# Kernel tuning notes

Measured on AMD Instinct MI355X. Metric: run time of the kernel, lower is better.

Reference implementation:

```python
import jax, jax.numpy as jnp
import numpy as np

V_NUM = 4
NUM_HEADS = 8


def setup_inputs() -> dict:
    key = jax.random.key(0)
    k1, k2, k3 = jax.random.split(key, 3)
    B, C, H, W = 8, 512, 24, 24
    x = jax.random.normal(k1, (B, C, H, W), dtype=jnp.float32)
    # 1x1 conv weights stored as [out_ch, in_ch]
    w_qkv = jax.random.normal(k2, (3 * C, C), dtype=jnp.float32) * (C ** -0.5)
    w_proj = jax.random.normal(k3, (C, C), dtype=jnp.float32) * (C ** -0.5)
    b_proj = jnp.zeros((C,), dtype=jnp.float32)
    return {"x": x, "w_qkv": w_qkv, "w_proj": w_proj, "b_proj": b_proj}


def reference(x, w_qkv, w_proj, b_proj):
    B, C, H, W = x.shape
    hd = C // NUM_HEADS          # head dim
    scale = hd ** -0.5
    g = B // V_NUM               # batch groups
    N = V_NUM * H * W            # tokens per group

    # 1x1 conv qkv (no bias): [B, 3C, H, W]
    qkv = jnp.einsum('bchw,oc->bohw', x, w_qkv)
    # [g, v, 3C, H, W] -> [g, 3C, v, H, W] -> [g, heads, 3*hd, N]
    t = qkv.reshape(g, V_NUM, 3 * C, H, W).transpose(0, 2, 1, 3, 4)
    t = t.reshape(g, NUM_HEADS, 3 * hd, N)
    q, k, v = jnp.split(t, 3, axis=2)  # each [g, heads, hd, N]

    # attn = k^T @ q * scale : [g, heads, N, N]
    attn = jnp.einsum('ghdn,ghdm->ghnm', k, q) * scale
    attn = jax.nn.softmax(attn, axis=-2)  # softmax over the k axis (dim=-2)

    # out = v @ attn : [g, heads, hd, N]
    out = jnp.einsum('ghdn,ghnm->ghdm', v, attn)
    # [g, C, v, H, W] -> [g, v, C, H, W] -> [B, C, H, W]
    out = out.reshape(g, C, V_NUM, H, W).transpose(0, 2, 1, 3, 4).reshape(B, C, H, W)

    # 1x1 conv proj with bias
    out = jnp.einsum('bchw,oc->bohw', out, w_proj) + b_proj[None, :, None, None]
    return out
```

## Files before the change

kernel.cpp:

```cpp
#include <hip/hip_runtime.h>
#include <stdint.h>

typedef _Float16 f16;
typedef _Float16 half8 __attribute__((ext_vector_type(8)));
typedef _Float16 half4 __attribute__((ext_vector_type(4)));
typedef float floatx4 __attribute__((ext_vector_type(4)));

#define LOG2E 1.44269504088896340736f

__device__ __forceinline__ void async_cp16(const void* g, void* l) {
  __builtin_amdgcn_global_load_lds((const __attribute__((address_space(1))) void*)g,
                                   (__attribute__((address_space(3))) void*)l, 16, 0, 0);
}

__global__ __launch_bounds__(256) void k_prep(const float* __restrict__ x,
                                              f16* __restrict__ XT,
                                              const float* __restrict__ wqkv,
                                              const float* __restrict__ wproj,
                                              f16* __restrict__ WQ, f16* __restrict__ WP) {
  __shared__ f16 sT[64][72];
  const int bid = blockIdx.x;
  const int tid = threadIdx.x;
  if (bid < 576) {
    const int hw0 = (bid % 9) * 64, c0 = ((bid / 9) & 7) * 64, b = bid / 72;
    const int cc = tid >> 6, hwc = tid & 63;
    const float* xb = x + (size_t)b * 294912;
    for (int i = 0; i < 16; ++i) {
      int c = c0 + i * 4 + cc;
      sT[hwc][i * 4 + cc] = (f16)xb[c * 576 + hw0 + hwc];
    }
    __syncthreads();
    const int c_c = tid & 63, rr = tid >> 6;
    f16* xtb = XT + ((size_t)b * 576 + hw0) * 512 + c0;
    for (int j = 0; j < 16; ++j) {
      int r = j * 4 + rr;
      xtb[(size_t)r * 512 + c_c] = sT[r][c_c];
    }
  } else {
    const float SCALE_Q = 0.125f * LOG2E;
    const int total1 = 1536 * 512, total2 = 512 * 512;
    for (int idx = (bid - 576) * 256 + tid; idx < total1 + total2; idx += 128 * 256) {
      if (idx < total1) {
        int row = idx >> 9;
        float v = wqkv[idx];
        if ((row % 192) < 64) v *= SCALE_Q;
        WQ[idx] = (f16)v;
      } else {
        WP[idx - total1] = (f16)wproj[idx - total1];
      }
    }
  }
}

__global__ __launch_bounds__(256) void k_qkv_gemm(const f16* __restrict__ XT,
                                                  const f16* __restrict__ WQ,
                                                  f16* __restrict__ Qh, f16* __restrict__ Kh,
                                                  f16* __restrict__ Vh) {
  const int t0 = blockIdx.x * 128, n0 = blockIdx.y * 128;
  __shared__ alignas(16) f16 smem[2 * 128 * 64];
  f16* sA = smem;
  f16* sB = smem + 128 * 64;
  const int tid = threadIdx.x;
  const int wave = tid >> 6, lane = tid & 63, quad = lane >> 4, l16 = lane & 15;
  const int msub = (wave & 1) * 64, nsub = (wave >> 1) * 64;
  const floatx4 fzero = {0.f, 0.f, 0.f, 0.f};
  floatx4 acc[4][4];
  for (int i = 0; i < 4; ++i)
    for (int j = 0; j < 4; ++j) acc[i][j] = fzero;

  for (int k0 = 0; k0 < 512; k0 += 64) {
    __syncthreads();
    for (int p = 0; p < 4; ++p) {
      int e = p * 256 + tid;
      int row = e >> 3, colb = e & 7;
      async_cp16((const char*)XT + ((size_t)(t0 + row) * 512 + k0 + colb * 8) * 2,
                 (char*)sA + e * 16);
      async_cp16((const char*)WQ + ((size_t)(n0 + row) * 512 + k0 + colb * 8) * 2,
                 (char*)sB + e * 16);
    }
    __syncthreads();
    for (int f = 0; f < 2; ++f) {
      half8 a[4], bfr[4];
      for (int ms = 0; ms < 4; ++ms)
        a[ms] = *(const half8*)&sA[(msub + ms * 16 + l16) * 64 + f * 32 + quad * 8];
      for (int ns = 0; ns < 4; ++ns)
        bfr[ns] = *(const half8*)&sB[(nsub + ns * 16 + l16) * 64 + f * 32 + quad * 8];
      for (int ms = 0; ms < 4; ++ms)
        for (int ns = 0; ns < 4; ++ns)
          acc[ms][ns] =
              __builtin_amdgcn_mfma_f32_16x16x32_f16(a[ms], bfr[ns], acc[ms][ns], 0, 0, 0);
    }
  }
  for (int ms = 0; ms < 4; ++ms) {
    int tbase = t0 + msub + ms * 16 + quad * 4;
    for (int ns = 0; ns < 4; ++ns) {
      int row = n0 + nsub + ns * 16 + l16;
      int h = row / 192, rr2 = row % 192;
      int sel = rr2 >> 6, d = rr2 & 63;
      if (sel == 2) continue;
      for (int r = 0; r < 4; ++r) {
        int t = tbase + r;
        int b = t / 576, hw = t % 576;
        int g = b >> 2, v = b & 3;
        int n = v * 576 + hw;
        int gh = g * 8 + h;
        f16 hv = (f16)acc[ms][ns][r];
        size_t idx = ((size_t)gh * 2304 + n) * 64 + d;
        if (sel == 0)
          Qh[idx] = hv;
        else
          Kh[idx] = hv;
      }
    }
  }
  const int r0 = n0 % 192;
  if (r0 != 0) {
    const int vloc = (r0 == 128) ? 0 : 64;
    const int h = (n0 + vloc) / 192;
    f16* sVT = smem;
    __syncthreads();
    if ((wave >> 1) == (vloc >> 6)) {
      for (int ms = 0; ms < 4; ++ms) {
        int tok = msub + ms * 16 + quad * 4;
        for (int ns = 0; ns < 4; ++ns) {
          int d = ns * 16 + l16;
          half4 hv;
          for (int r = 0; r < 4; ++r) hv[r] = (f16)acc[ms][ns][r];
          *(half4*)&sVT[d * 136 + tok] = hv;
        }
      }
    }
    __syncthreads();
    for (int pss = 0; pss < 4; ++pss) {
      int d = pss * 16 + (tid >> 4), chunk = tid & 15;
      int t = t0 + chunk * 8;
      int b = t / 576, hw = t - b * 576;
      int gh = (b >> 2) * 8 + h, n = (b & 3) * 576 + hw;
      *(half8*)(Vh + (size_t)gh * 147456 + (size_t)d * 2304 + n) =
          *(const half8*)&sVT[d * 136 + chunk * 8];
    }
  }
}

__global__ __launch_bounds__(256) void k_attn(const f16* __restrict__ Qh,
                                              const f16* __restrict__ Kh,
                                              const f16* __restrict__ Vh,
                                              f16* __restrict__ AOT) {
  const int mt = blockIdx.x, gh = blockIdx.y;
  const int m0 = mt * 64;
  const int g = gh >> 3, h = gh & 7;
  const f16* Qg = Qh + (size_t)gh * 147456;
  const f16* Kg = Kh + (size_t)gh * 147456;
  const f16* Vg = Vh + (size_t)gh * 147456;
  __shared__ alignas(16) f16 sK[2][2][64 * 64];
  __shared__ alignas(16) f16 sV[2][2][64 * 64];
  const int tid = threadIdx.x;
  const int wave = tid >> 6, lane = tid & 63, quad = lane >> 4, l16 = lane & 15;
  const int wq = wave & 1, half = wave >> 1;
  const floatx4 fzero = {0.f, 0.f, 0.f, 0.f};
  const int sw = l16 & 7;

  auto stage_kv = [&](int ktile, int buf) {
#pragma unroll
    for (int p = 0; p < 8; ++p) {
      const int half_t = (p >> 1) & 1, isV = p >> 2;
      int idx = (p & 1) * 256 + tid;
      int row = idx >> 3, cb = idx & 7, sc = ((cb ^ (row & 7)) << 3);
      int nb = half_t * 1152 + ktile * 64;
      if (!isV)
        async_cp16(Kg + (size_t)(nb + row) * 64 + sc, (char*)&sK[half_t][buf][0] + idx * 16);
      else
        async_cp16(Vg + (size_t)row * 2304 + nb + sc, (char*)&sV[half_t][buf][0] + idx * 16);
    }
  };

  half8 qa[2][2];
  for (int s = 0; s < 2; ++s) {
    int qrow = m0 + wq * 32 + s * 16 + l16;
    qa[s][0] = *(const half8*)(Qg + (size_t)qrow * 64 + quad * 8);
    qa[s][1] = *(const half8*)(Qg + (size_t)qrow * 64 + 32 + quad * 8);
  }

  stage_kv(0, 0);
  __syncthreads();
  stage_kv(1, 1);

  float l_lane[2] = {0.f, 0.f};
  floatx4 o[2][4];
  for (int s = 0; s < 2; ++s)
    for (int dt = 0; dt < 4; ++dt) o[s][dt] = fzero;

  for (int kt = 0; kt < 18; ++kt) {
    const f16* bK = &sK[half][kt & 1][0];
    const f16* bV = &sV[half][kt & 1][0];

    half4 pf[2][4];
#pragma unroll
    for (int nt = 0; nt < 4; ++nt) {
      int krow = nt * 16 + l16;
      half8 kb0 = *(const half8*)&bK[krow * 64 + ((quad ^ sw) << 3)];
      half8 kb1 = *(const half8*)&bK[krow * 64 + (((4 + quad) ^ sw) << 3)];
#pragma unroll
      for (int s = 0; s < 2; ++s) {
        floatx4 t = __builtin_amdgcn_mfma_f32_16x16x32_f16(kb0, qa[s][0], fzero, 0, 0, 0);
        t = __builtin_amdgcn_mfma_f32_16x16x32_f16(kb1, qa[s][1], t, 0, 0, 0);
#pragma unroll
        for (int r = 0; r < 4; ++r) {
          float e = __builtin_amdgcn_exp2f(t[r]);
          l_lane[s] += e;
          pf[s][nt][r] = (f16)e;
        }
      }
    }
#pragma unroll
    for (int dt = 0; dt < 4; ++dt) {
      int vrow = dt * 16 + l16;
#pragma unroll
      for (int nt = 0; nt < 4; ++nt) {
        int chunk = nt * 2 + (quad >> 1);
        half4 vb = *(const half4*)&bV[vrow * 64 + ((chunk ^ sw) << 3) + (quad & 1) * 4];
#pragma unroll
        for (int s = 0; s < 2; ++s)
          o[s][dt] = __builtin_amdgcn_mfma_f32_16x16x16f16(pf[s][nt], vb, o[s][dt], 0, 0, 0);
      }
    }

    if (kt < 17) {
      __syncthreads();
      if (kt + 2 < 18) stage_kv(kt + 2, kt & 1);
    }
  }

  __syncthreads();
  float* cO = (float*)sK;
  float* cL = (float*)sV;
  if (half == 1) {
    for (int s = 0; s < 2; ++s) {
      cL[(wq * 2 + s) * 64 + lane] = l_lane[s];
      for (int dt = 0; dt < 4; ++dt)
        *(floatx4*)&cO[((((wq * 2 + s) * 4 + dt) * 64 + lane) * 4)] = o[s][dt];
    }
  }
  __syncthreads();
  if (half == 0) {
    for (int s = 0; s < 2; ++s) {
      l_lane[s] += cL[(wq * 2 + s) * 64 + lane];
      for (int dt = 0; dt < 4; ++dt)
        o[s][dt] += *(const floatx4*)&cO[((((wq * 2 + s) * 4 + dt) * 64 + lane) * 4)];
    }
    for (int s = 0; s < 2; ++s) {
      l_lane[s] += __shfl_xor(l_lane[s], 16, 64);
      l_lane[s] += __shfl_xor(l_lane[s], 32, 64);
      float inv[4];
      for (int r = 0; r < 4; ++r) {
        float lr = __shfl(l_lane[s], quad * 4 + r, 64);
        inv[r] = 1.f / lr;
      }
      for (int dt = 0; dt < 4; ++dt)
        for (int r = 0; r < 4; ++r) {
          int n_tok = m0 + wq * 32 + s * 16 + quad * 4 + r;
          int v = n_tok / 576, hw = n_tok % 576;
          int bb = g * 4 + v;
          int c = h * 64 + dt * 16 + l16;
          AOT[((size_t)bb * 576 + hw) * 512 + c] = (f16)(o[s][dt][r] * inv[r]);
        }
    }
  }
}

__global__ __launch_bounds__(256) void k_proj_gemm(const f16* __restrict__ AOT,
                                                   const f16* __restrict__ WP,
                                                   const float* __restrict__ bias,
                                                   float* __restrict__ out) {
  const int o0 = blockIdx.x * 64, t0 = blockIdx.y * 128;
  __shared__ alignas(16) f16 sA[64 * 64];
  __shared__ alignas(16) f16 sB[128 * 64];
  const int tid = threadIdx.x;
  const int wave = tid >> 6, lane = tid & 63, quad = lane >> 4, l16 = lane & 15;
  const int msub = (wave & 1) * 32, nsub = (wave >> 1) * 64;
  const floatx4 fzero = {0.f, 0.f, 0.f, 0.f};
  floatx4 acc[2][4];
  for (int i = 0; i < 2; ++i)
    for (int j = 0; j < 4; ++j) acc[i][j] = fzero;

  for (int k0 = 0; k0 < 512; k0 += 64) {
    __syncthreads();
    for (int p = 0; p < 2; ++p) {
      int e = p * 256 + tid;
      int row = e >> 3, colb = e & 7;
      async_cp16((const char*)WP + ((size_t)(o0 + row) * 512 + k0 + colb * 8) * 2,
                 (char*)sA + e * 16);
    }
    for (int p = 0; p < 4; ++p) {
      int e = p * 256 + tid;
      int row = e >> 3, colb = e & 7;
      async_cp16((const char*)AOT + ((size_t)(t0 + row) * 512 + k0 + colb * 8) * 2,
                 (char*)sB + e * 16);
    }
    __syncthreads();
    for (int f = 0; f < 2; ++f) {
      half8 a[2], bfr[4];
      for (int ms = 0; ms < 2; ++ms)
        a[ms] = *(const half8*)&sA[(msub + ms * 16 + l16) * 64 + f * 32 + quad * 8];
      for (int ns = 0; ns < 4; ++ns)
        bfr[ns] = *(const half8*)&sB[(nsub + ns * 16 + l16) * 64 + f * 32 + quad * 8];
      for (int ms = 0; ms < 2; ++ms)
        for (int ns = 0; ns < 4; ++ns)
          acc[ms][ns] =
              __builtin_amdgcn_mfma_f32_16x16x32_f16(a[ms], bfr[ns], acc[ms][ns], 0, 0, 0);
    }
  }
  for (int ms = 0; ms < 2; ++ms) {
    int o_row = o0 + msub + ms * 16 + quad * 4;
    for (int ns = 0; ns < 4; ++ns) {
      int t = t0 + nsub + ns * 16 + l16;
      int b = t / 576, hw = t % 576;
      for (int r = 0; r < 4; ++r) {
        int orow = o_row + r;
        out[(size_t)b * 294912 + (size_t)orow * 576 + hw] = acc[ms][ns][r] + bias[orow];
      }
    }
  }
}

extern "C" void kernel_launch(void* const* d_in, const int* in_sizes, int n_in,
                              void* d_out, int out_size, void* d_ws, size_t ws_size,
                              hipStream_t stream) {
  const float* x = (const float*)d_in[0];
  const float* wqkv = (const float*)d_in[1];
  const float* wproj = (const float*)d_in[2];
  const float* bias = (const float*)d_in[3];
  float* out = (float*)d_out;
  char* ws = (char*)d_ws;
  f16* XT = (f16*)(ws + 0);
  f16* WQ = (f16*)(ws + 4718592);
  f16* WP = (f16*)(ws + 6291456);
  f16* Qh = (f16*)(ws + 6815744);
  f16* Kh = (f16*)(ws + 11534336);
  f16* Vh = (f16*)(ws + 16252928);
  f16* AOT = (f16*)(ws + 20971520);

  k_prep<<<dim3(704), dim3(256), 0, stream>>>(x, XT, wqkv, wproj, WQ, WP);
  k_qkv_gemm<<<dim3(36, 12), dim3(256), 0, stream>>>(XT, WQ, Qh, Kh, Vh);
  k_attn<<<dim3(36, 16), dim3(256), 0, stream>>>(Qh, Kh, Vh, AOT);
  k_proj_gemm<<<dim3(8, 36), dim3(256), 0, stream>>>(AOT, WP, bias, out);
}
```

Measured before the change: 154.3 us.

## Split attention key range across four wave groups with 512-thread blocks

The attention kernel grows from 256 to 512 threads, so the 2304-key range is split into four quarters of 32-key tiles instead of two halves of 64-key tiles. The shared-memory staging layout and V swizzle are changed to fit 32-wide tiles, and the final reduction merges partial sums from three wave groups instead of one. The aim is more waves per block to hide latency and shorten each wave's serial key loop. In exchange the cross-wave reduction grows, each wave does less work per barrier, and register pressure under the larger launch bound could limit occupancy.

```diff
diff --git a/kernel.cpp b/kernel.cpp
--- a/kernel.cpp
+++ b/kernel.cpp
@@ -142,7 +142,7 @@
   }
 }
 
-__global__ __launch_bounds__(256) void k_attn(const f16* __restrict__ Qh,
+__global__ __launch_bounds__(512) void k_attn(const f16* __restrict__ Qh,
                                               const f16* __restrict__ Kh,
                                               const f16* __restrict__ Vh,
                                               f16* __restrict__ AOT) {
@@ -152,29 +152,37 @@
   const f16* Qg = Qh + (size_t)gh * 147456;
   const f16* Kg = Kh + (size_t)gh * 147456;
   const f16* Vg = Vh + (size_t)gh * 147456;
-  __shared__ alignas(16) f16 sK[2][2][64 * 64];
-  __shared__ alignas(16) f16 sV[2][2][64 * 64];
+  __shared__ alignas(16) f16 smem[32768];
+  f16* sK = smem;
+  f16* sV = smem + 16384;
   const int tid = threadIdx.x;
   const int wave = tid >> 6, lane = tid & 63, quad = lane >> 4, l16 = lane & 15;
-  const int wq = wave & 1, half = wave >> 1;
+  const int wq = wave & 1, qtr = wave >> 1;
   const floatx4 fzero = {0.f, 0.f, 0.f, 0.f};
   const int sw = l16 & 7;
+  const int vsw = (l16 >> 1) & 3;
 
   auto stage_kv = [&](int ktile, int buf) {
 #pragma unroll
-    for (int p = 0; p < 8; ++p) {
-      const int half_t = (p >> 1) & 1, isV = p >> 2;
-      int idx = (p & 1) * 256 + tid;
-      int row = idx >> 3, cb = idx & 7, sc = ((cb ^ (row & 7)) << 3);
-      int nb = half_t * 1152 + ktile * 64;
-      if (!isV)
-        async_cp16(Kg + (size_t)(nb + row) * 64 + sc, (char*)&sK[half_t][buf][0] + idx * 16);
-      else
-        async_cp16(Vg + (size_t)row * 2304 + nb + sc, (char*)&sV[half_t][buf][0] + idx * 16);
+    for (int p = 0; p < 4; ++p) {
+      int idx = p * 512 + tid;
+      int rem = idx & 1023;
+      int qt = rem >> 8, unit = rem & 255;
+      if (idx < 1024) {
+        int row = unit >> 3, cb = unit & 7;
+        async_cp16(Kg + (size_t)(qt * 576 + ktile * 32 + row) * 64 + ((cb ^ (row & 7)) << 3),
+                   (char*)(sK + (qt * 2 + buf) * 2048) + unit * 16);
+      } else {
+        int row = unit >> 2, cb = unit & 3;
+        async_cp16(
+            Vg + (size_t)row * 2304 + qt * 576 + ktile * 32 + ((cb ^ ((row >> 1) & 3)) << 3),
+            (char*)(sV + (qt * 2 + buf) * 2048) + unit * 16);
+      }
     }
   };
 
   half8 qa[2][2];
+#pragma unroll
   for (int s = 0; s < 2; ++s) {
     int qrow = m0 + wq * 32 + s * 16 + l16;
     qa[s][0] = *(const half8*)(Qg + (size_t)qrow * 64 + quad * 8);
@@ -191,12 +199,12 @@
     for (int dt = 0; dt < 4; ++dt) o[s][dt] = fzero;
 
   for (int kt = 0; kt < 18; ++kt) {
-    const f16* bK = &sK[half][kt & 1][0];
-    const f16* bV = &sV[half][kt & 1][0];
-
-    half4 pf[2][4];
-#pragma unroll
-    for (int nt = 0; nt < 4; ++nt) {
+    const f16* bK = sK + (qtr * 2 + (kt & 1)) * 2048;
+    const f16* bV = sV + (qtr * 2 + (kt & 1)) * 2048;
+
+    half4 pf[2][2];
+#pragma unroll
+    for (int nt = 0; nt < 2; ++nt) {
       int krow = nt * 16 + l16;
       half8 kb0 = *(const half8*)&bK[krow * 64 + ((quad ^ sw) << 3)];
       half8 kb1 = *(const half8*)&bK[krow * 64 + (((4 + quad) ^ sw) << 3)];
@@ -216,9 +224,9 @@
     for (int dt = 0; dt < 4; ++dt) {
       int vrow = dt * 16 + l16;
 #pragma unroll
-      for (int nt = 0; nt < 4; ++nt) {
+      for (int nt = 0; nt < 2; ++nt) {
         int chunk = nt * 2 + (quad >> 1);
-        half4 vb = *(const half4*)&bV[vrow * 64 + ((chunk ^ sw) << 3) + (quad & 1) * 4];
+        half4 vb = *(const half4*)&bV[vrow * 32 + ((chunk ^ vsw) << 3) + (quad & 1) * 4];
 #pragma unroll
         for (int s = 0; s < 2; ++s)
           o[s][dt] = __builtin_amdgcn_mfma_f32_16x16x16f16(pf[s][nt], vb, o[s][dt], 0, 0, 0);
@@ -232,21 +240,27 @@
   }
 
   __syncthreads();
-  float* cO = (float*)sK;
-  float* cL = (float*)sV;
-  if (half == 1) {
+  float* cO = (float*)smem;
+  float* cL = (float*)(smem + 24576);
+  if (qtr != 0) {
+    int base = (qtr - 1) * 2 + wq;
+#pragma unroll
     for (int s = 0; s < 2; ++s) {
-      cL[(wq * 2 + s) * 64 + lane] = l_lane[s];
+      cL[(base * 2 + s) * 64 + lane] = l_lane[s];
       for (int dt = 0; dt < 4; ++dt)
-        *(floatx4*)&cO[((((wq * 2 + s) * 4 + dt) * 64 + lane) * 4)] = o[s][dt];
+        *(floatx4*)&cO[(((base * 2 + s) * 4 + dt) * 64 + lane) * 4] = o[s][dt];
     }
   }
   __syncthreads();
-  if (half == 0) {
-    for (int s = 0; s < 2; ++s) {
-      l_lane[s] += cL[(wq * 2 + s) * 64 + lane];
-      for (int dt = 0; dt < 4; ++dt)
-        o[s][dt] += *(const floatx4*)&cO[((((wq * 2 + s) * 4 + dt) * 64 + lane) * 4)];
+  if (qtr == 0) {
+#pragma unroll
+    for (int q2 = 0; q2 < 3; ++q2) {
+      int base = q2 * 2 + wq;
+      for (int s = 0; s < 2; ++s) {
+        l_lane[s] += cL[(base * 2 + s) * 64 + lane];
+        for (int dt = 0; dt < 4; ++dt)
+          o[s][dt] += *(const floatx4*)&cO[(((base * 2 + s) * 4 + dt) * 64 + lane) * 4];
+      }
     }
     for (int s = 0; s < 2; ++s) {
       l_lane[s] += __shfl_xor(l_lane[s], 16, 64);
@@ -342,6 +356,6 @@
 
   k_prep<<<dim3(704), dim3(256), 0, stream>>>(x, XT, wqkv, wproj, WQ, WP);
   k_qkv_gemm<<<dim3(36, 12), dim3(256), 0, stream>>>(XT, WQ, Qh, Kh, Vh);
-  k_attn<<<dim3(36, 16), dim3(256), 0, stream>>>(Qh, Kh, Vh, AOT);
+  k_attn<<<dim3(36, 16), dim3(512), 0, stream>>>(Qh, Kh, Vh, AOT);
   k_proj_gemm<<<dim3(8, 36), dim3(256), 0, stream>>>(AOT, WP, bias, out);
 }
```

Result: faster. 151.0 us (-2.2%).
